# Optimization experiments

Hardware: AMD Instinct MI355X
Metric: run time of the kernel (lower is better)

The kernel has to match this reference:

```python
import jax, jax.numpy as jnp
import numpy as np

N = 50000      # num nodes
E = 1600000    # num edges
C = 128        # channels
F = 4          # number of framelet filters
K = 6          # Chebyshev order
S = 1.0        # spectral scale s
APPROX = np.array([[0.3, 0.15, 0.1, 0.075, 0.06, 0.05],
                   [0.6, 0.3, 0.2, 0.15, 0.12, 0.1],
                   [0.9, 0.45, 0.3, 0.225, 0.18, 0.15],
                   [1.2, 0.6, 0.4, 0.3, 0.24, 0.2]], dtype=np.float32)


def setup_inputs() -> dict:
    key = jax.random.key(0)
    ks = jax.random.split(key, 6)
    scale = (2.0 / C) ** 0.5
    return {
        "x_real": jax.random.normal(ks[0], (N, C), jnp.float32),
        "x_imag": jax.random.normal(ks[1], (N, C), jnp.float32),
        "edge_index": jax.random.randint(ks[2], (2, E), 0, N, dtype=jnp.int32),
        "edge_weight": jax.random.uniform(ks[3], (E,), jnp.float32),
        "approx": jnp.asarray(APPROX),
        "theta": jnp.ones((F,), jnp.float32),
        "W_r": jax.random.normal(ks[4], (C, C), jnp.float32) * scale,
        "W_i": jax.random.normal(ks[5], (C, C), jnp.float32) * scale,
        "num_nodes": N,
    }


def _framelet_fwd(x_real, x_imag, edge_index, edge_weight, approx, theta, W_r, W_i, num_nodes):
    row, col = edge_index[0], edge_index[1]
    w = edge_weight / S

    def A_norm(h):  # h: [N, C] real; normalized adjacency propagation
        return jax.ops.segment_sum(w[:, None] * h[col], row, num_segments=num_nodes)

    # Linearity: sum_i theta_i * sum_k approx[i,k] * T_k(x) == sum_k c_k * T_k(x)
    c = theta @ approx  # [K] effective Chebyshev coefficients

    T0r, T0i = x_real, x_imag
    out_r = c[0] * T0r
    out_i = c[0] * T0i
    T1r, T1i = -A_norm(T0r), -A_norm(T0i)
    out_r = out_r + c[1] * T1r
    out_i = out_i + c[1] * T1i
    for ki in range(2, K):
        T2r = -2.0 * A_norm(T1r) - T0r
        T2i = -2.0 * A_norm(T1i) - T0i
        out_r = out_r + c[ki] * T2r
        out_i = out_i + c[ki] * T2i
        T0r, T0i, T1r, T1i = T1r, T1i, T2r, T2i

    # complex linear: (r + i*j) @ (W_r + W_i*j)^T
    yr = out_r @ W_r.T - out_i @ W_i.T
    yi = out_r @ W_i.T + out_i @ W_r.T
    # CSiLU: SiLU applied to real/imag parts independently
    return jnp.stack([jax.nn.silu(yr), jax.nn.silu(yi)])  # [2, N, C]


def reference(x_real, x_imag, edge_index, edge_weight, approx, theta, W_r, W_i, num_nodes):
    return _framelet_fwd(x_real, x_imag, edge_index, edge_weight, approx, theta, W_r, W_i, num_nodes)
```

## Files before the change

kernel.cpp:

```cpp
#include <hip/hip_runtime.h>
#include <hip/hip_fp16.h>
#include <math.h>


#define CH   128
#define NP   128
#define NP4  64
#define RPB  128
#define MAXBUCK 512

typedef _Float16 half8 __attribute__((ext_vector_type(8)));
typedef float f32x4 __attribute__((ext_vector_type(4)));

__device__ __forceinline__ uint2 ntload_u2(const uint2* p) {
    unsigned long long v = __builtin_nontemporal_load((const unsigned long long*)p);
    uint2 r; r.x = (unsigned)v; r.y = (unsigned)(v >> 32);
    return r;
}


__global__ __launch_bounds__(256) void bucket_hist_k(
        const int* __restrict__ row, int* __restrict__ bucket_cnt, int E, int nbuck) {
    __shared__ int h[MAXBUCK];
    for (int j = threadIdx.x; j < nbuck; j += 256) h[j] = 0;
    __syncthreads();
    int stride = gridDim.x * 256;
    for (int e = blockIdx.x * 256 + threadIdx.x; e < E; e += stride)
        atomicAdd(&h[row[e] >> 7], 1);
    __syncthreads();
    for (int j = threadIdx.x; j < nbuck; j += 256)
        if (h[j]) atomicAdd(&bucket_cnt[j], h[j]);
}

__global__ __launch_bounds__(512) void bucket_scan_k(
        const int* __restrict__ bucket_cnt, int* __restrict__ bucket_start,
        int* __restrict__ bucket_cursor, int nbuck, int E) {
    __shared__ int sd[MAXBUCK];
    int t = threadIdx.x;
    int v = (t < nbuck) ? bucket_cnt[t] : 0;
    sd[t] = v;
    __syncthreads();
    for (int off = 1; off < MAXBUCK; off <<= 1) {
        int y = (t >= off) ? sd[t - off] : 0;
        __syncthreads();
        sd[t] += y;
        __syncthreads();
    }
    int excl = sd[t] - v;
    if (t < nbuck) { bucket_start[t] = excl; bucket_cursor[t] = excl; }
    if (t == 0) bucket_start[nbuck] = E;
}

__global__ __launch_bounds__(256) void bucket_place_k(
        const int* __restrict__ row, const int* __restrict__ col,
        const float* __restrict__ w, int* __restrict__ bucket_cursor,
        uint2* __restrict__ tmp, int E, int chunk, int nbuck) {
    __shared__ int cnt[MAXBUCK];
    __shared__ int cur[MAXBUCK];
    int e0 = blockIdx.x * chunk;
    int e1 = e0 + chunk; if (e1 > E) e1 = E;
    if (e0 >= E) return;
    for (int j = threadIdx.x; j < nbuck; j += 256) cnt[j] = 0;
    __syncthreads();
    for (int e = e0 + threadIdx.x; e < e1; e += 256)
        atomicAdd(&cnt[row[e] >> 7], 1);
    __syncthreads();
    for (int j = threadIdx.x; j < nbuck; j += 256) {
        int c = cnt[j];
        cur[j] = c ? atomicAdd(&bucket_cursor[j], c) : 0;
    }
    __syncthreads();
    for (int e = e0 + threadIdx.x; e < e1; e += 256) {
        int r = row[e];
        int b = r >> 7;
        int p = atomicAdd(&cur[b], 1);
        uint2 ent;
        ent.x = ((unsigned)(r & (RPB - 1)) << 16) | (unsigned)col[e];
        ent.y = __float_as_uint(w[e]);
        tmp[p] = ent;
    }
}

__global__ __launch_bounds__(256) void csr_build_k(
        const uint2* __restrict__ tmp, const int* __restrict__ bucket_start,
        int* __restrict__ row_start, unsigned* __restrict__ csr4,
        int N, int E, int nbuck) {
    __shared__ int hist[RPB];
    __shared__ int sc[RPB];
    __shared__ int curs[RPB];
    int b = blockIdx.x;
    int t = threadIdx.x;
    int base = bucket_start[b];
    int endp = bucket_start[b + 1];
    if (t < RPB) hist[t] = 0;
    __syncthreads();
    for (int e = base + t; e < endp; e += 256)
        atomicAdd(&hist[tmp[e].x >> 16], 1);
    __syncthreads();
    if (t < RPB) sc[t] = hist[t];
    __syncthreads();
    for (int off = 1; off < RPB; off <<= 1) {
        int y = 0;
        if (t < RPB && t >= off) y = sc[t - off];
        __syncthreads();
        if (t < RPB) sc[t] += y;
        __syncthreads();
    }
    int r0 = b << 7;
    if (t < RPB) {
        int excl = sc[t] - hist[t];
        if (r0 + t < N) row_start[r0 + t] = base + excl;
        curs[t] = base + excl;
    }
    if (b == nbuck - 1 && t == 0) row_start[N] = E;
    __syncthreads();
    for (int e = base + t; e < endp; e += 256) {
        uint2 ent = tmp[e];
        int rl = ent.x >> 16;
        unsigned c = ent.x & 0xffffu;
        float wv = __uint_as_float(ent.y) * (-1.0f / 16.0f);
        int p = atomicAdd(&curs[rl], 1);
        __half hw = __float2half(wv);
        csr4[p] = (c << 16) | (unsigned)__half_as_ushort(hw);
    }
}

__global__ void coef_k(const float* __restrict__ approx, const float* __restrict__ theta,
                       float* cp) {
    int k = threadIdx.x;
    if (k < 6 && blockIdx.x == 0) {
        float s = 0.f;
        for (int f = 0; f < 4; f++) s += theta[f] * approx[f * 6 + k];
        float sc = 1.f;
        for (int j = 0; j < k; j++) sc *= 32.f;
        cp[k] = s * sc;
    }
}

__global__ void convert_x_k(const float2* __restrict__ xr2, const float2* __restrict__ xi2,
                            __half2* __restrict__ xbuf, int total) {
    int idx = blockIdx.x * blockDim.x + threadIdx.x;
    if (idx >= total) return;
    int i = idx >> 7;
    int p = idx & 127;
    float2 v = (p < 64) ? xr2[(size_t)i * 64 + p] : xi2[(size_t)i * 64 + (p - 64)];
    xbuf[idx] = __floats2half2_rn(v.x, v.y);
}

__global__ void build_whT_k(const float* __restrict__ Wr, const float* __restrict__ Wi,
                            _Float16* __restrict__ WhT) {
    int idx = blockIdx.x * 256 + threadIdx.x;
    int j = idx >> 8, k = idx & 255;
    float v;
    if (j < 128) {
        v = (k < 128) ? Wr[j * 128 + k] : -Wi[j * 128 + (k - 128)];
    } else {
        v = (k < 128) ? Wi[(j - 128) * 128 + k] : Wr[(j - 128) * 128 + (k - 128)];
    }
    WhT[idx] = (_Float16)v;
}


__device__ __forceinline__ void unpack4(uint2 v, float& a, float& b, float& c, float& d) {
    __half2 lo = *reinterpret_cast<__half2*>(&v.x);
    __half2 hi = *reinterpret_cast<__half2*>(&v.y);
    float2 f0 = __half22float2(lo);
    float2 f1 = __half22float2(hi);
    a = f0.x; b = f0.y; c = f1.x; d = f1.y;
}

__device__ __forceinline__ void decode(unsigned ent, int& c, float& wv) {
    c = (int)(ent >> 16);
    wv = __half2float(__ushort_as_half((unsigned short)(ent & 0xffffu)));
}

__device__ __forceinline__ void gather_row(
        const uint2* __restrict__ src, const unsigned* __restrict__ csr,
        int beg, int end, int slot,
        float& s0, float& s1, float& s2, float& s3) {
    int e = beg;
    unsigned c0, c1, c2, c3;
    if (e + 4 <= end) { c0 = csr[e]; c1 = csr[e+1]; c2 = csr[e+2]; c3 = csr[e+3]; }
    for (; e + 8 <= end; e += 4) {
        unsigned n0 = csr[e+4], n1 = csr[e+5], n2 = csr[e+6], n3 = csr[e+7];
        int ia, ib, ic, id; float wa, wb, wc, wd;
        decode(c0, ia, wa); decode(c1, ib, wb); decode(c2, ic, wc); decode(c3, id, wd);
        float a0,a1,a2,a3, b0,b1,b2,b3, d0,d1,d2,d3, f0,f1,f2,f3;
        unpack4(src[(size_t)ia * NP4 + slot], a0,a1,a2,a3);
        unpack4(src[(size_t)ib * NP4 + slot], b0,b1,b2,b3);
        unpack4(src[(size_t)ic * NP4 + slot], d0,d1,d2,d3);
        unpack4(src[(size_t)id * NP4 + slot], f0,f1,f2,f3);
        s0 += wa*a0 + wb*b0 + wc*d0 + wd*f0;
        s1 += wa*a1 + wb*b1 + wc*d1 + wd*f1;
        s2 += wa*a2 + wb*b2 + wc*d2 + wd*f2;
        s3 += wa*a3 + wb*b3 + wc*d3 + wd*f3;
        c0 = n0; c1 = n1; c2 = n2; c3 = n3;
    }
    if (e + 4 <= end) {
        int ia, ib, ic, id; float wa, wb, wc, wd;
        decode(c0, ia, wa); decode(c1, ib, wb); decode(c2, ic, wc); decode(c3, id, wd);
        float a0,a1,a2,a3, b0,b1,b2,b3, d0,d1,d2,d3, f0,f1,f2,f3;
        unpack4(src[(size_t)ia * NP4 + slot], a0,a1,a2,a3);
        unpack4(src[(size_t)ib * NP4 + slot], b0,b1,b2,b3);
        unpack4(src[(size_t)ic * NP4 + slot], d0,d1,d2,d3);
        unpack4(src[(size_t)id * NP4 + slot], f0,f1,f2,f3);
        s0 += wa*a0 + wb*b0 + wc*d0 + wd*f0;
        s1 += wa*a1 + wb*b1 + wc*d1 + wd*f1;
        s2 += wa*a2 + wb*b2 + wc*d2 + wd*f2;
        s3 += wa*a3 + wb*b3 + wc*d3 + wd*f3;
        e += 4;
    }
    for (; e < end; e++) {
        int ia; float wa;
        decode(csr[e], ia, wa);
        float a0,a1,a2,a3;
        unpack4(src[(size_t)ia * NP4 + slot], a0,a1,a2,a3);
        s0 += wa*a0; s1 += wa*a1; s2 += wa*a2; s3 += wa*a3;
    }
}

__global__ __launch_bounds__(256) void spmm_first4_k(
        const uint2* __restrict__ xb4,
        const int* __restrict__ row_start, const unsigned* __restrict__ csr,
        uint2* __restrict__ dst, int N) {
    int blk = blockIdx.x;
    int c = blk & 1;
    int rb = blk >> 1;
    int t = threadIdx.x;
    int rl = t >> 5;
    int p4 = t & 31;
    int i = rb * 8 + rl;
    if (i >= N) return;
    int slot = c * 32 + p4;
    int beg = row_start[i], end = row_start[i + 1];
    float s0 = 0.f, s1 = 0.f, s2 = 0.f, s3 = 0.f;
    gather_row(xb4, csr, beg, end, slot, s0, s1, s2, s3);
    s0 *= 0.5f; s1 *= 0.5f; s2 *= 0.5f; s3 *= 0.5f;
    uint2 pk;
    __half2 h0 = __floats2half2_rn(s0, s1);
    __half2 h1 = __floats2half2_rn(s2, s3);
    pk.x = *reinterpret_cast<unsigned*>(&h0);
    pk.y = *reinterpret_cast<unsigned*>(&h1);
    dst[(size_t)i * NP4 + slot] = pk;
}

__global__ __launch_bounds__(256) void spmm_step4_k(
        const uint2* __restrict__ cur, const uint2* __restrict__ prev,
        const int* __restrict__ row_start, const unsigned* __restrict__ csr,
        uint2* __restrict__ dst, int N) {
    int blk = blockIdx.x;
    int c = blk & 1;
    int rb = blk >> 1;
    int t = threadIdx.x;
    int rl = t >> 5;
    int p4 = t & 31;
    int i = rb * 8 + rl;
    if (i >= N) return;
    int slot = c * 32 + p4;
    int beg = row_start[i], end = row_start[i + 1];
    float s0 = 0.f, s1 = 0.f, s2 = 0.f, s3 = 0.f;
    gather_row(cur, csr, beg, end, slot, s0, s1, s2, s3);
    float p0,p1,p2,p3;
    unpack4(ntload_u2(&prev[(size_t)i * NP4 + slot]), p0,p1,p2,p3);
    const float inv = 1.0f / 1024.0f;
    float t0 = s0 - inv * p0;
    float t1v = s1 - inv * p1;
    float t2v = s2 - inv * p2;
    float t3v = s3 - inv * p3;
    uint2 pk;
    __half2 h0 = __floats2half2_rn(t0, t1v);
    __half2 h1 = __floats2half2_rn(t2v, t3v);
    pk.x = *reinterpret_cast<unsigned*>(&h0);
    pk.y = *reinterpret_cast<unsigned*>(&h1);
    dst[(size_t)i * NP4 + slot] = pk;
}

__global__ __launch_bounds__(256) void gemm_silu_mfma_k(
        const _Float16* __restrict__ WhT,
        const uint2* __restrict__ x0, const uint2* __restrict__ t1b,
        const uint2* __restrict__ t2b, const uint2* __restrict__ t3b,
        const float* __restrict__ cp,
        float* __restrict__ out, int N) {
    __shared__ _Float16 U[32][264];
    int t = threadIdx.x;
    int row0 = blockIdx.x * 32;
    const uint2* t4b = (const uint2*)out;
    const uint2* t5b = (const uint2*)out + (size_t)N * NP4;
    const float isc = 1.0f / 32.0f;
    float w0 = cp[0], w1 = cp[1], w2 = cp[2], w3 = cp[3], w4 = cp[4], w5 = cp[5];
    for (int q = t; q < 2048; q += 256) {
        int r = q >> 6;
        int s = q & 63;
        int row = row0 + r;
        float a0 = 0.f, a1 = 0.f, a2 = 0.f, a3 = 0.f;
        if (row < N) {
            size_t idx = (size_t)row * NP4 + s;
            float v0,v1,v2,v3;
            unpack4(ntload_u2(&x0[idx]),  v0,v1,v2,v3);
            a0 += w0*v0; a1 += w0*v1; a2 += w0*v2; a3 += w0*v3;
            unpack4(ntload_u2(&t1b[idx]), v0,v1,v2,v3);
            a0 += w1*v0; a1 += w1*v1; a2 += w1*v2; a3 += w1*v3;
            unpack4(ntload_u2(&t2b[idx]), v0,v1,v2,v3);
            a0 += w2*v0; a1 += w2*v1; a2 += w2*v2; a3 += w2*v3;
            unpack4(ntload_u2(&t3b[idx]), v0,v1,v2,v3);
            a0 += w3*v0; a1 += w3*v1; a2 += w3*v2; a3 += w3*v3;
            unpack4(ntload_u2(&t4b[idx]), v0,v1,v2,v3);
            a0 += w4*v0; a1 += w4*v1; a2 += w4*v2; a3 += w4*v3;
            unpack4(ntload_u2(&t5b[idx]), v0,v1,v2,v3);
            a0 += w5*v0; a1 += w5*v1; a2 += w5*v2; a3 += w5*v3;
        }
        int k = s * 4;
        U[r][k]   = (_Float16)(a0 * isc);
        U[r][k+1] = (_Float16)(a1 * isc);
        U[r][k+2] = (_Float16)(a2 * isc);
        U[r][k+3] = (_Float16)(a3 * isc);
    }
    __syncthreads();

    int wave = t >> 6;
    int lane = t & 63;
    int colbase = wave * 64;
    int lr = lane & 15;
    int lg = lane >> 4;
    f32x4 acc[2][4] = {};
    for (int kb = 0; kb < 8; kb++) {
        int k0 = kb * 32 + lg * 8;
        half8 a0 = *(const half8*)&U[lr][k0];
        half8 a1 = *(const half8*)&U[16 + lr][k0];
        #pragma unroll
        for (int nf = 0; nf < 4; nf++) {
            int col = colbase + nf * 16 + lr;
            half8 b = *(const half8*)&WhT[(size_t)col * 256 + k0];
            acc[0][nf] = __builtin_amdgcn_mfma_f32_16x16x32_f16(a0, b, acc[0][nf], 0, 0, 0);
            acc[1][nf] = __builtin_amdgcn_mfma_f32_16x16x32_f16(a1, b, acc[1][nf], 0, 0, 0);
        }
    }

    #pragma unroll
    for (int mf = 0; mf < 2; mf++) {
        #pragma unroll
        for (int nf = 0; nf < 4; nf++) {
            int col = colbase + nf * 16 + lr;
            int half = col >> 7, j = col & 127;
            #pragma unroll
            for (int r4 = 0; r4 < 4; r4++) {
                int row = row0 + mf * 16 + lg * 4 + r4;
                if (row < N) {
                    float v = acc[mf][nf][r4] * 32.f;
                    float sv = v / (1.f + expf(-v));
                    out[(size_t)half * N * CH + (size_t)row * CH + j] = sv;
                }
            }
        }
    }
}


extern "C" void kernel_launch(void* const* d_in, const int* in_sizes, int n_in,
                              void* d_out, int out_size, void* d_ws, size_t ws_size,
                              hipStream_t stream) {
    const float* xr     = (const float*)d_in[0];
    const float* xi     = (const float*)d_in[1];
    const int*   eidx   = (const int*)d_in[2];
    const float* ew     = (const float*)d_in[3];
    const float* approx = (const float*)d_in[4];
    const float* theta  = (const float*)d_in[5];
    const float* Wr     = (const float*)d_in[6];
    const float* Wi     = (const float*)d_in[7];

    const int N = in_sizes[0] / CH;
    const int E = in_sizes[3];
    const int* rowv = eidx;
    const int* colv = eidx + E;

    float* outp = (float*)d_out;

    char* w8 = (char*)d_ws;
    size_t off = 0;
    auto alloc = [&](size_t bytes) -> void* {
        void* ptr = w8 + off;
        off += (bytes + 255) & ~(size_t)255;
        return ptr;
    };
    float*    cp        = (float*)alloc(64 * 4);
    int*      bucket_cnt= (int*)alloc(MAXBUCK * 4);
    int*      bucket_st = (int*)alloc((MAXBUCK + 1) * 4);
    int*      bucket_cur= (int*)alloc(MAXBUCK * 4);
    int*      row_start = (int*)alloc((size_t)(N + 1) * 4);
    unsigned* csr4      = (unsigned*)alloc((size_t)E * 4);
    _Float16* WhT       = (_Float16*)alloc(256 * 256 * 2);
    uint2*    xbuf      = (uint2*)alloc((size_t)N * NP4 * 8);
    uint2*    T1        = (uint2*)alloc((size_t)N * NP4 * 8);
    uint2*    T2        = (uint2*)alloc((size_t)N * NP4 * 8);
    uint2*    T3        = (uint2*)alloc((size_t)N * NP4 * 8);
    uint2*    tmp       = T3;
    uint2*    T4        = (uint2*)d_out;
    uint2*    T5        = (uint2*)d_out + (size_t)N * NP4;
    (void)ws_size;

    const int nbuck = (N + RPB - 1) / RPB;
    const int chunk = (E + 255) / 256;
    const int NH = N * NP;

    hipMemsetAsync(bucket_cnt, 0, (size_t)MAXBUCK * 4, stream);
    coef_k<<<1, 64, 0, stream>>>(approx, theta, cp);
    build_whT_k<<<256, 256, 0, stream>>>(Wr, Wi, WhT);
    bucket_hist_k<<<256, 256, 0, stream>>>(rowv, bucket_cnt, E, nbuck);
    bucket_scan_k<<<1, MAXBUCK, 0, stream>>>(bucket_cnt, bucket_st, bucket_cur, nbuck, E);
    bucket_place_k<<<256, 256, 0, stream>>>(rowv, colv, ew, bucket_cur, tmp, E, chunk, nbuck);
    csr_build_k<<<nbuck, 256, 0, stream>>>(tmp, bucket_st, row_start, csr4, N, E, nbuck);
    convert_x_k<<<(NH + 255) / 256, 256, 0, stream>>>(
        (const float2*)xr, (const float2*)xi, (__half2*)xbuf, NH);

    const int NG = 2 * ((N + 7) / 8);

    spmm_first4_k<<<NG, 256, 0, stream>>>(xbuf, row_start, csr4, T1, N);
    spmm_step4_k<<<NG, 256, 0, stream>>>(T1, xbuf, row_start, csr4, T2, N);
    spmm_step4_k<<<NG, 256, 0, stream>>>(T2, T1, row_start, csr4, T3, N);
    spmm_step4_k<<<NG, 256, 0, stream>>>(T3, T2, row_start, csr4, T4, N);
    spmm_step4_k<<<NG, 256, 0, stream>>>(T4, T3, row_start, csr4, T5, N);

    gemm_silu_mfma_k<<<(N + 31) / 32, 256, 0, stream>>>(
        WhT, xbuf, T1, T2, T3, cp, outp, N);
}
```

Baseline: 603.5 us.

## Sort rows by degree for load-balanced SpMM scheduling

Adds a counting sort of rows by degree (histogram, scan, scatter) that produces a permuted list of row begin/end/original index, largest degree first. The SpMM kernels then iterate over this permuted order so rows of similar length land in the same block, reducing imbalance between the 32-lane row groups in a block. In exchange it adds three small kernels plus a memset, an extra indirection per row, and scattered output writes, since destination rows are no longer contiguous per block. With uniform random edges the degree spread is narrow (mean around 32), so the benefit may be limited.

Result: slower. 696.9 us (+15.5%).

```diff
diff --git a/kernel.cpp b/kernel.cpp
--- a/kernel.cpp
+++ b/kernel.cpp
@@ -123,6 +123,51 @@
         __half hw = __float2half(wv);
         csr4[p] = (c << 16) | (unsigned)__half_as_ushort(hw);
     }
+}
+
+
+__device__ __forceinline__ int row_key(int d) {
+    if (d > 255) d = 255;
+    return 255 - d;
+}
+
+__global__ __launch_bounds__(256) void row_hist_k(
+        const int* __restrict__ row_start, int* __restrict__ rh, int N) {
+    __shared__ int h[256];
+    h[threadIdx.x] = 0;
+    __syncthreads();
+    int stride = gridDim.x * 256;
+    for (int i = blockIdx.x * 256 + threadIdx.x; i < N; i += stride)
+        atomicAdd(&h[row_key(row_start[i + 1] - row_start[i])], 1);
+    __syncthreads();
+    if (h[threadIdx.x]) atomicAdd(&rh[threadIdx.x], h[threadIdx.x]);
+}
+
+__global__ __launch_bounds__(256) void row_scan_k(
+        const int* __restrict__ rh, int* __restrict__ rcur) {
+    __shared__ int sd[256];
+    int t = threadIdx.x;
+    int v = rh[t];
+    sd[t] = v;
+    __syncthreads();
+    for (int off = 1; off < 256; off <<= 1) {
+        int y = (t >= off) ? sd[t - off] : 0;
+        __syncthreads();
+        sd[t] += y;
+        __syncthreads();
+    }
+    rcur[t] = sd[t] - v;
+}
+
+__global__ __launch_bounds__(256) void row_scatter_k(
+        const int* __restrict__ row_start, int* __restrict__ rcur,
+        int* __restrict__ sbeg, int* __restrict__ send, int* __restrict__ sorig,
+        int N) {
+    int i = blockIdx.x * 256 + threadIdx.x;
+    if (i >= N) return;
+    int a = row_start[i], b = row_start[i + 1];
+    int q = atomicAdd(&rcur[row_key(b - a)], 1);
+    sbeg[q] = a; send[q] = b; sorig[q] = i;
 }
 
 __global__ void coef_k(const float* __restrict__ approx, const float* __restrict__ theta,
@@ -221,7 +266,8 @@
 
 __global__ __launch_bounds__(256) void spmm_first4_k(
         const uint2* __restrict__ xb4,
-        const int* __restrict__ row_start, const unsigned* __restrict__ csr,
+        const int* __restrict__ sbeg, const int* __restrict__ send,
+        const int* __restrict__ sorig, const unsigned* __restrict__ csr,
         uint2* __restrict__ dst, int N) {
     int blk = blockIdx.x;
     int c = blk & 1;
@@ -229,10 +275,11 @@
     int t = threadIdx.x;
     int rl = t >> 5;
     int p4 = t & 31;
-    int i = rb * 8 + rl;
-    if (i >= N) return;
+    int p = rb * 8 + rl;
+    if (p >= N) return;
     int slot = c * 32 + p4;
-    int beg = row_start[i], end = row_start[i + 1];
+    int beg = sbeg[p], end = send[p];
+    int i = sorig[p];
     float s0 = 0.f, s1 = 0.f, s2 = 0.f, s3 = 0.f;
     gather_row(xb4, csr, beg, end, slot, s0, s1, s2, s3);
     s0 *= 0.5f; s1 *= 0.5f; s2 *= 0.5f; s3 *= 0.5f;
@@ -246,7 +293,8 @@
 
 __global__ __launch_bounds__(256) void spmm_step4_k(
         const uint2* __restrict__ cur, const uint2* __restrict__ prev,
-        const int* __restrict__ row_start, const unsigned* __restrict__ csr,
+        const int* __restrict__ sbeg, const int* __restrict__ send,
+        const int* __restrict__ sorig, const unsigned* __restrict__ csr,
         uint2* __restrict__ dst, int N) {
     int blk = blockIdx.x;
     int c = blk & 1;
@@ -254,10 +302,11 @@
     int t = threadIdx.x;
     int rl = t >> 5;
     int p4 = t & 31;
-    int i = rb * 8 + rl;
-    if (i >= N) return;
+    int p = rb * 8 + rl;
+    if (p >= N) return;
     int slot = c * 32 + p4;
-    int beg = row_start[i], end = row_start[i + 1];
+    int beg = sbeg[p], end = send[p];
+    int i = sorig[p];
     float s0 = 0.f, s1 = 0.f, s2 = 0.f, s3 = 0.f;
     gather_row(cur, csr, beg, end, slot, s0, s1, s2, s3);
     float p0,p1,p2,p3;
@@ -341,14 +390,14 @@
         #pragma unroll
         for (int nf = 0; nf < 4; nf++) {
             int col = colbase + nf * 16 + lr;
-            int half = col >> 7, j = col & 127;
+            int half = col >> 7, jj = col & 127;
             #pragma unroll
             for (int r4 = 0; r4 < 4; r4++) {
                 int row = row0 + mf * 16 + lg * 4 + r4;
                 if (row < N) {
                     float v = acc[mf][nf][r4] * 32.f;
                     float sv = v / (1.f + expf(-v));
-                    out[(size_t)half * N * CH + (size_t)row * CH + j] = sv;
+                    out[(size_t)half * N * CH + (size_t)row * CH + jj] = sv;
                 }
             }
         }
@@ -386,7 +435,12 @@
     int*      bucket_cnt= (int*)alloc(MAXBUCK * 4);
     int*      bucket_st = (int*)alloc((MAXBUCK + 1) * 4);
     int*      bucket_cur= (int*)alloc(MAXBUCK * 4);
+    int*      rh        = (int*)alloc(256 * 4);
+    int*      rcur      = (int*)alloc(256 * 4);
     int*      row_start = (int*)alloc((size_t)(N + 1) * 4);
+    int*      sbeg      = (int*)alloc((size_t)N * 4);
+    int*      send      = (int*)alloc((size_t)N * 4);
+    int*      sorig     = (int*)alloc((size_t)N * 4);
     unsigned* csr4      = (unsigned*)alloc((size_t)E * 4);
     _Float16* WhT       = (_Float16*)alloc(256 * 256 * 2);
     uint2*    xbuf      = (uint2*)alloc((size_t)N * NP4 * 8);
@@ -403,22 +457,27 @@
     const int NH = N * NP;
 
     hipMemsetAsync(bucket_cnt, 0, (size_t)MAXBUCK * 4, stream);
+    hipMemsetAsync(rh, 0, 256 * 4, stream);
     coef_k<<<1, 64, 0, stream>>>(approx, theta, cp);
     build_whT_k<<<256, 256, 0, stream>>>(Wr, Wi, WhT);
     bucket_hist_k<<<256, 256, 0, stream>>>(rowv, bucket_cnt, E, nbuck);
     bucket_scan_k<<<1, MAXBUCK, 0, stream>>>(bucket_cnt, bucket_st, bucket_cur, nbuck, E);
     bucket_place_k<<<256, 256, 0, stream>>>(rowv, colv, ew, bucket_cur, tmp, E, chunk, nbuck);
     csr_build_k<<<nbuck, 256, 0, stream>>>(tmp, bucket_st, row_start, csr4, N, E, nbuck);
+    row_hist_k<<<128, 256, 0, stream>>>(row_start, rh, N);
+    row_scan_k<<<1, 256, 0, stream>>>(rh, rcur);
+    row_scatter_k<<<(N + 255) / 256, 256, 0, stream>>>(
+        row_start, rcur, sbeg, send, sorig, N);
     convert_x_k<<<(NH + 255) / 256, 256, 0, stream>>>(
         (const float2*)xr, (const float2*)xi, (__half2*)xbuf, NH);
 
     const int NG = 2 * ((N + 7) / 8);
 
-    spmm_first4_k<<<NG, 256, 0, stream>>>(xbuf, row_start, csr4, T1, N);
-    spmm_step4_k<<<NG, 256, 0, stream>>>(T1, xbuf, row_start, csr4, T2, N);
-    spmm_step4_k<<<NG, 256, 0, stream>>>(T2, T1, row_start, csr4, T3, N);
-    spmm_step4_k<<<NG, 256, 0, stream>>>(T3, T2, row_start, csr4, T4, N);
-    spmm_step4_k<<<NG, 256, 0, stream>>>(T4, T3, row_start, csr4, T5, N);
+    spmm_first4_k<<<NG, 256, 0, stream>>>(xbuf, sbeg, send, sorig, csr4, T1, N);
+    spmm_step4_k<<<NG, 256, 0, stream>>>(T1, xbuf, sbeg, send, sorig, csr4, T2, N);
+    spmm_step4_k<<<NG, 256, 0, stream>>>(T2, T1, sbeg, send, sorig, csr4, T3, N);
+    spmm_step4_k<<<NG, 256, 0, stream>>>(T3, T2, sbeg, send, sorig, csr4, T4, N);
+    spmm_step4_k<<<NG, 256, 0, stream>>>(T4, T3, sbeg, send, sorig, csr4, T5, N);
 
     gemm_silu_mfma_k<<<(N + 31) / 32, 256, 0, stream>>>(
         WhT, xbuf, T1, T2, T3, cp, outp, N);
```
